# Kernel optimization log

Measured on AMD Instinct MI355X. Metric: run time of the kernel, lower is better.

## Reference

```python
import jax, jax.numpy as jnp
import numpy as np

N_NODES = 100000
N_EDGES = 500000
IN_DIM = 128
OUT_DIM = 128
NUM_HEADS = 4
HEAD_DIM = OUT_DIM // NUM_HEADS  # 32


def setup_inputs() -> dict:
    key = jax.random.key(0)
    k1, k2, k3, k4, k5, k6 = jax.random.split(key, 6)
    features = jax.random.normal(k1, (N_NODES, IN_DIM), dtype=jnp.float32)
    edge_index = jax.random.randint(k2, (2, N_EDGES), 0, N_NODES, dtype=jnp.int64)
    W_lin = jax.random.normal(k3, (OUT_DIM, IN_DIM), dtype=jnp.float32) * 0.05
    b_lin = jax.random.normal(k4, (OUT_DIM,), dtype=jnp.float32) * 0.05
    W_att = jax.random.normal(k5, (NUM_HEADS, 2 * OUT_DIM), dtype=jnp.float32) * 0.05
    b_att = jax.random.normal(k6, (NUM_HEADS,), dtype=jnp.float32) * 0.05
    return {"features": features, "edge_index": edge_index,
            "W_lin": W_lin, "b_lin": b_lin, "W_att": W_att, "b_att": b_att}


def reference(features, edge_index, W_lin, b_lin, W_att, b_att):
    num_nodes = features.shape[0]
    h = features @ W_lin.T + b_lin                     # [N, D]
    src, dst = edge_index[0], edge_index[1]
    src_h = h[src]                                     # [E, D]
    dst_h = h[dst]                                     # [E, D]
    # attention = Linear(cat([src_h, dst_h])) without materializing the concat
    logits = src_h @ W_att[:, :OUT_DIM].T + dst_h @ W_att[:, OUT_DIM:].T + b_att  # [E, H]
    # original softmaxes over dim=0 (all edges), per head
    attn = jax.nn.softmax(logits, axis=0)              # [E, H]
    # FAITHFUL quirk: only the first head_dim columns of src_h feed every head
    msgs = src_h[:, None, :HEAD_DIM] * attn[:, :, None]  # [E, H, head_dim]
    agg = jax.ops.segment_sum(msgs.reshape(msgs.shape[0], -1), dst,
                              num_segments=num_nodes)  # [N, H*head_dim] head-major
    return agg + h                                     # dropout(p=0) is identity
```

## Files before the change

### kernel.cpp

```cpp
#include <hip/hip_runtime.h>
#include <hip/hip_bf16.h>
#include <stdint.h>

#define N_NODES  100000
#define N_EDGES  500000
#define DIM      128
#define NUM_HEADS 4
#define HEAD_DIM  32
#define CAP      28

#define C_BLOCKS ((N_EDGES + 255) / 256)

typedef __attribute__((ext_vector_type(8))) __bf16 bf16x8;
typedef __attribute__((ext_vector_type(4))) __bf16 bf16x4;
typedef __attribute__((ext_vector_type(4))) float  f32x4;

__device__ __forceinline__ bf16x8 cvt8(const float* __restrict__ p)
{
    const float4 lo = *reinterpret_cast<const float4*>(p);
    const float4 hi = *reinterpret_cast<const float4*>(p + 4);
    bf16x8 r;
    r[0] = (__bf16)lo.x; r[1] = (__bf16)lo.y; r[2] = (__bf16)lo.z; r[3] = (__bf16)lo.w;
    r[4] = (__bf16)hi.x; r[5] = (__bf16)hi.y; r[6] = (__bf16)hi.z; r[7] = (__bf16)hi.w;
    return r;
}

__device__ __forceinline__ unsigned pack2_bf16(float a, float b)
{
    const __bf16 ba = (__bf16)a, bb = (__bf16)b;
    const unsigned short ua = __builtin_bit_cast(unsigned short, ba);
    const unsigned short ub = __builtin_bit_cast(unsigned short, bb);
    return (unsigned)ua | ((unsigned)ub << 16);
}

__device__ __forceinline__ float unpack_bf16(unsigned p, int hi)
{
    const unsigned short u = (unsigned short)(hi ? (p >> 16) : p);
    const __bf16 b = __builtin_bit_cast(__bf16, u);
    return (float)b;
}

__global__ __launch_bounds__(256) void cvt_wlin_kernel(
    const float* __restrict__ Wlin,
    __bf16* __restrict__ wb)
{
    const int i = blockIdx.x * 256 + threadIdx.x;
    const float4 v = *reinterpret_cast<const float4*>(Wlin + (size_t)i * 4);
    bf16x4 o;
    o[0] = (__bf16)v.x; o[1] = (__bf16)v.y; o[2] = (__bf16)v.z; o[3] = (__bf16)v.w;
    *reinterpret_cast<bf16x4*>(wb + (size_t)i * 4) = o;
}

__global__ __launch_bounds__(256) void gemm_dots_kernel(
    const float* __restrict__ feat,
    const __bf16* __restrict__ wb,
    const float* __restrict__ blin,
    const float* __restrict__ Watt,
    float* __restrict__ h,
    __bf16* __restrict__ h32,
    float* __restrict__ a_src,
    float* __restrict__ a_dst)
{
    __shared__ float wl[1280];
    const int tid = threadIdx.x;
#pragma unroll
    for (int i = 0; i < 4; ++i) {
        const int t  = tid + i * 256;
        const int hd = t >> 8;
        const int cf = t & 255;
        const int c  = cf & 127;
        const int df = cf >> 7;
        wl[c * 10 + df * 4 + hd] = Watt[t];
    }
    __syncthreads();

    const int wv   = tid >> 6;
    const int lane = tid & 63;
    const int wave = blockIdx.x * 4 + wv;
    const int m    = lane & 15;
    const int quad = lane >> 4;
    const int node0 = wave * 16;
    if (node0 >= N_NODES) return;

    f32x4 acc[8];
#pragma unroll
    for (int jt = 0; jt < 8; ++jt) acc[jt] = (f32x4){0.f, 0.f, 0.f, 0.f};

#pragma unroll
    for (int kc = 0; kc < 4; ++kc) {
        bf16x8 a = cvt8(feat + (size_t)(node0 + m) * DIM + kc * 32 + quad * 8);
#pragma unroll
        for (int jt = 0; jt < 8; ++jt) {
            bf16x8 b = *reinterpret_cast<const bf16x8*>(
                wb + ((jt * 16 + m) << 7) + kc * 32 + quad * 8);
            acc[jt] = __builtin_amdgcn_mfma_f32_16x16x32_bf16(a, b, acc[jt], 0, 0, 0);
        }
    }

    float dsrc[16], ddst[16];
#pragma unroll
    for (int i = 0; i < 16; ++i) { dsrc[i] = 0.f; ddst[i] = 0.f; }

#pragma unroll
    for (int jt = 0; jt < 8; ++jt) {
        const int col = jt * 16 + m;
        const float bl = blin[col];
        float w[8];
        *reinterpret_cast<float2*>(&w[0]) = *reinterpret_cast<const float2*>(&wl[col * 10 + 0]);
        *reinterpret_cast<float2*>(&w[2]) = *reinterpret_cast<const float2*>(&wl[col * 10 + 2]);
        *reinterpret_cast<float2*>(&w[4]) = *reinterpret_cast<const float2*>(&wl[col * 10 + 4]);
        *reinterpret_cast<float2*>(&w[6]) = *reinterpret_cast<const float2*>(&wl[col * 10 + 6]);
#pragma unroll
        for (int r = 0; r < 4; ++r) {
            const float hv = acc[jt][r] + bl;
            const int row = node0 + quad * 4 + r;
            h[(size_t)row * DIM + col] = hv;
            if (jt < 2)
                h32[(size_t)row * HEAD_DIM + col] = (__bf16)hv;
            dsrc[r * 4 + 0] += hv * w[0];
            dsrc[r * 4 + 1] += hv * w[1];
            dsrc[r * 4 + 2] += hv * w[2];
            dsrc[r * 4 + 3] += hv * w[3];
            ddst[r * 4 + 0] += hv * w[4];
            ddst[r * 4 + 1] += hv * w[5];
            ddst[r * 4 + 2] += hv * w[6];
            ddst[r * 4 + 3] += hv * w[7];
        }
    }

#pragma unroll
    for (int off = 1; off <= 8; off <<= 1) {
#pragma unroll
        for (int i = 0; i < 16; ++i) {
            dsrc[i] += __shfl_xor(dsrc[i], off, 64);
            ddst[i] += __shfl_xor(ddst[i], off, 64);
        }
    }
    if (m == 0) {
#pragma unroll
        for (int r = 0; r < 4; ++r) {
            const int node = node0 + quad * 4 + r;
            float4 s = {dsrc[r * 4 + 0], dsrc[r * 4 + 1], dsrc[r * 4 + 2], dsrc[r * 4 + 3]};
            float4 d = {ddst[r * 4 + 0], ddst[r * 4 + 1], ddst[r * 4 + 2], ddst[r * 4 + 3]};
            *reinterpret_cast<float4*>(a_src + (size_t)node * 4) = s;
            *reinterpret_cast<float4*>(a_dst + (size_t)node * 4) = d;
        }
    }
}

__global__ __launch_bounds__(256) void edge_exp_bucket_kernel(
    const int* __restrict__ ei,
    const float* __restrict__ a_src,
    const float* __restrict__ a_dst,
    const float* __restrict__ batt,
    float* __restrict__ partials,
    int* __restrict__ cursor,
    int4* __restrict__ slots)
{
    __shared__ float lds[4][4];
    const int e = blockIdx.x * 256 + threadIdx.x;
    const int wv = threadIdx.x >> 6;
    const int lane = threadIdx.x & 63;
    float ex0 = 0.f, ex1 = 0.f, ex2 = 0.f, ex3 = 0.f;
    if (e < N_EDGES) {
        const int s = ei[e];
        const int d = ei[N_EDGES + e];
        const float4 as = *reinterpret_cast<const float4*>(a_src + (size_t)s * 4);
        const float4 ad = *reinterpret_cast<const float4*>(a_dst + (size_t)d * 4);
        ex0 = __expf(as.x + ad.x + batt[0]);
        ex1 = __expf(as.y + ad.y + batt[1]);
        ex2 = __expf(as.z + ad.z + batt[2]);
        ex3 = __expf(as.w + ad.w + batt[3]);
        const int pos = atomicAdd(&cursor[d], 1);
        if (pos < CAP) {
            int4 q;
            q.x = s;
            q.y = (int)pack2_bf16(ex0, ex1);
            q.z = (int)pack2_bf16(ex2, ex3);
            q.w = 0;
            slots[(size_t)d * CAP + pos] = q;
        }
    }
#pragma unroll
    for (int off = 32; off > 0; off >>= 1) {
        ex0 += __shfl_xor(ex0, off, 64);
        ex1 += __shfl_xor(ex1, off, 64);
        ex2 += __shfl_xor(ex2, off, 64);
        ex3 += __shfl_xor(ex3, off, 64);
    }
    if (lane == 0) {
        lds[wv][0] = ex0; lds[wv][1] = ex1; lds[wv][2] = ex2; lds[wv][3] = ex3;
    }
    __syncthreads();
    if (threadIdx.x < 4) {
        const float s = lds[0][threadIdx.x] + lds[1][threadIdx.x]
                      + lds[2][threadIdx.x] + lds[3][threadIdx.x];
        atomicAdd(&partials[(blockIdx.x & 7) * 4 + threadIdx.x], s);
    }
}

__global__ __launch_bounds__(256) void aggregate_kernel(
    const float* __restrict__ h,
    const __bf16* __restrict__ h32,
    const float* __restrict__ partials,
    const int* __restrict__ cursor,
    const int4* __restrict__ slots,
    float* __restrict__ out)
{
    const int nv = blockIdx.x * 4 + (threadIdx.x >> 6);
    const int lane = threadIdx.x & 63;
    if (nv >= N_NODES) return;
    const int n = __builtin_amdgcn_readfirstlane(nv);

    const int hd0 = lane >> 5;
    const int dd  = lane & 31;

    const float hn0 = h[(size_t)n * DIM + lane];
    const float hn1 = h[(size_t)n * DIM + 64 + lane];
    const int cnt_raw = cursor[n];

    const float4* __restrict__ p4 = reinterpret_cast<const float4*>(partials);
    float Sx = 0.f, Sy = 0.f, Sz = 0.f, Sw = 0.f;
#pragma unroll
    for (int b = 0; b < 8; ++b) {
        const float4 t = p4[b];
        Sx += t.x; Sy += t.y; Sz += t.z; Sw += t.w;
    }
    const float inv0 = 1.0f / (hd0 ? Sy : Sx);
    const float inv1 = 1.0f / (hd0 ? Sw : Sz);

    const int cnt = cnt_raw > CAP ? CAP : cnt_raw;
    const int4* __restrict__ sl = slots + (size_t)n * CAP;

    float acc0 = 0.f, acc1 = 0.f;
    int j = 0;
    for (; j + 4 <= cnt; j += 4) {
        const int4 q0 = sl[j];
        const int4 q1 = sl[j + 1];
        const int4 q2 = sl[j + 2];
        const int4 q3 = sl[j + 3];
        const float v0 = (float)h32[(size_t)q0.x * HEAD_DIM + dd];
        const float v1 = (float)h32[(size_t)q1.x * HEAD_DIM + dd];
        const float v2 = (float)h32[(size_t)q2.x * HEAD_DIM + dd];
        const float v3 = (float)h32[(size_t)q3.x * HEAD_DIM + dd];
        acc0 += v0 * unpack_bf16((unsigned)q0.y, hd0);
        acc1 += v0 * unpack_bf16((unsigned)q0.z, hd0);
        acc0 += v1 * unpack_bf16((unsigned)q1.y, hd0);
        acc1 += v1 * unpack_bf16((unsigned)q1.z, hd0);
        acc0 += v2 * unpack_bf16((unsigned)q2.y, hd0);
        acc1 += v2 * unpack_bf16((unsigned)q2.z, hd0);
        acc0 += v3 * unpack_bf16((unsigned)q3.y, hd0);
        acc1 += v3 * unpack_bf16((unsigned)q3.z, hd0);
    }
    for (; j < cnt; ++j) {
        const int4 q = sl[j];
        const float v = (float)h32[(size_t)q.x * HEAD_DIM + dd];
        acc0 += v * unpack_bf16((unsigned)q.y, hd0);
        acc1 += v * unpack_bf16((unsigned)q.z, hd0);
    }
    out[(size_t)n * DIM + lane]      = acc0 * inv0 + hn0;
    out[(size_t)n * DIM + 64 + lane] = acc1 * inv1 + hn1;
}

extern "C" void kernel_launch(void* const* d_in, const int* in_sizes, int n_in,
                              void* d_out, int out_size, void* d_ws, size_t ws_size,
                              hipStream_t stream)
{
    const float* feat = (const float*)d_in[0];
    const int*   ei   = (const int*)d_in[1];
    const float* Wlin = (const float*)d_in[2];
    const float* blin = (const float*)d_in[3];
    const float* Watt = (const float*)d_in[4];
    const float* batt = (const float*)d_in[5];
    float*       out  = (float*)d_out;

    const size_t NF = (size_t)N_NODES * DIM;
    float*  h        = (float*)d_ws;
    float*  a_src    = h + NF;
    float*  a_dst    = a_src + (size_t)N_NODES * 4;
    int*    cursor   = (int*)(a_dst + (size_t)N_NODES * 4);
    float*  partials = (float*)(cursor + N_NODES);
    int4*   slots    = (int4*)(partials + 32);
    __bf16* h32      = (__bf16*)(slots + (size_t)N_NODES * CAP);
    __bf16* wlin_bf  = h32 + (size_t)N_NODES * HEAD_DIM;

    hipMemsetAsync(cursor, 0, (size_t)N_NODES * sizeof(int) + 32 * sizeof(float), stream);

    cvt_wlin_kernel<<<16, 256, 0, stream>>>(Wlin, wlin_bf);
    gemm_dots_kernel<<<1563, 256, 0, stream>>>(feat, wlin_bf, blin, Watt,
                                               h, h32, a_src, a_dst);
    edge_exp_bucket_kernel<<<C_BLOCKS, 256, 0, stream>>>(ei, a_src, a_dst, batt,
                                                         partials, cursor, slots);
    aggregate_kernel<<<25000, 256, 0, stream>>>(h, h32, partials, cursor, slots, out);
}
```

Measured before the change: 210.9 us.

## Restructure linear-layer GEMM with fragment-ordered weights and transposed MFMA output

The bf16 weight conversion now writes W_lin in the exact MFMA fragment order, so each lane loads one contiguous bf16x8 per tile. Each 16-node group is split across two waves that each compute half of the output columns. The MFMA operands are swapped so each lane holds four consecutive columns of a single node, which allows float4 stores of h and bf16x4 stores of h32 instead of scattered scalar stores. The attention dot reductions shrink to two shuffles plus an LDS combine across the two waves, at the cost of an extra block barrier and twice as many waves per node.

```diff
diff --git a/kernel.cpp b/kernel.cpp
--- a/kernel.cpp
+++ b/kernel.cpp
@@ -10,6 +10,7 @@
 #define CAP      28
 
 #define C_BLOCKS ((N_EDGES + 255) / 256)
+#define G_BLOCKS (N_NODES / 32)
 
 typedef __attribute__((ext_vector_type(8))) __bf16 bf16x8;
 typedef __attribute__((ext_vector_type(4))) __bf16 bf16x4;
@@ -44,11 +45,13 @@
     const float* __restrict__ Wlin,
     __bf16* __restrict__ wb)
 {
-    const int i = blockIdx.x * 256 + threadIdx.x;
-    const float4 v = *reinterpret_cast<const float4*>(Wlin + (size_t)i * 4);
-    bf16x4 o;
-    o[0] = (__bf16)v.x; o[1] = (__bf16)v.y; o[2] = (__bf16)v.z; o[3] = (__bf16)v.w;
-    *reinterpret_cast<bf16x4*>(wb + (size_t)i * 4) = o;
+    const int t    = blockIdx.x * 256 + threadIdx.x;
+    const int jt   = t >> 8;
+    const int kc   = (t >> 6) & 3;
+    const int quad = (t >> 4) & 3;
+    const int m    = t & 15;
+    const bf16x8 o = cvt8(Wlin + (size_t)(jt * 16 + m) * DIM + kc * 32 + quad * 8);
+    *reinterpret_cast<bf16x8*>(wb + (size_t)t * 8) = o;
 }
 
 __global__ __launch_bounds__(256) void gemm_dots_kernel(
@@ -62,6 +65,8 @@
     float* __restrict__ a_dst)
 {
     __shared__ float wl[1280];
+    __shared__ float bl_l[128];
+    __shared__ float sm[2][2][16][8];
     const int tid = threadIdx.x;
 #pragma unroll
     for (int i = 0; i < 4; ++i) {
@@ -72,79 +77,96 @@
         const int df = cf >> 7;
         wl[c * 10 + df * 4 + hd] = Watt[t];
     }
+    if (tid < 128) bl_l[tid] = blin[tid];
     __syncthreads();
 
     const int wv   = tid >> 6;
+    const int g    = wv >> 1;
+    const int ch   = wv & 1;
     const int lane = tid & 63;
-    const int wave = blockIdx.x * 4 + wv;
     const int m    = lane & 15;
     const int quad = lane >> 4;
-    const int node0 = wave * 16;
-    if (node0 >= N_NODES) return;
-
-    f32x4 acc[8];
-#pragma unroll
-    for (int jt = 0; jt < 8; ++jt) acc[jt] = (f32x4){0.f, 0.f, 0.f, 0.f};
+    const int node0 = (blockIdx.x * 2 + g) * 16;
+    const int node  = node0 + m;
+
+    f32x4 acc[4];
+#pragma unroll
+    for (int jtl = 0; jtl < 4; ++jtl) acc[jtl] = (f32x4){0.f, 0.f, 0.f, 0.f};
+
+    const bf16x8* __restrict__ wf =
+        reinterpret_cast<const bf16x8*>(wb) + (size_t)ch * 16 * 64 + lane;
 
 #pragma unroll
     for (int kc = 0; kc < 4; ++kc) {
-        bf16x8 a = cvt8(feat + (size_t)(node0 + m) * DIM + kc * 32 + quad * 8);
-#pragma unroll
-        for (int jt = 0; jt < 8; ++jt) {
-            bf16x8 b = *reinterpret_cast<const bf16x8*>(
-                wb + ((jt * 16 + m) << 7) + kc * 32 + quad * 8);
-            acc[jt] = __builtin_amdgcn_mfma_f32_16x16x32_bf16(a, b, acc[jt], 0, 0, 0);
-        }
-    }
-
-    float dsrc[16], ddst[16];
-#pragma unroll
-    for (int i = 0; i < 16; ++i) { dsrc[i] = 0.f; ddst[i] = 0.f; }
-
-#pragma unroll
-    for (int jt = 0; jt < 8; ++jt) {
-        const int col = jt * 16 + m;
-        const float bl = blin[col];
-        float w[8];
-        *reinterpret_cast<float2*>(&w[0]) = *reinterpret_cast<const float2*>(&wl[col * 10 + 0]);
-        *reinterpret_cast<float2*>(&w[2]) = *reinterpret_cast<const float2*>(&wl[col * 10 + 2]);
-        *reinterpret_cast<float2*>(&w[4]) = *reinterpret_cast<const float2*>(&wl[col * 10 + 4]);
-        *reinterpret_cast<float2*>(&w[6]) = *reinterpret_cast<const float2*>(&wl[col * 10 + 6]);
+        const bf16x8 a = cvt8(feat + (size_t)node * DIM + kc * 32 + quad * 8);
+#pragma unroll
+        for (int jtl = 0; jtl < 4; ++jtl) {
+            const bf16x8 b = wf[(jtl * 4 + kc) * 64];
+            acc[jtl] = __builtin_amdgcn_mfma_f32_16x16x32_bf16(b, a, acc[jtl], 0, 0, 0);
+        }
+    }
+
+    float dsrc[4] = {0.f, 0.f, 0.f, 0.f};
+    float ddst[4] = {0.f, 0.f, 0.f, 0.f};
+
+#pragma unroll
+    for (int jtl = 0; jtl < 4; ++jtl) {
+        const int jtg  = ch * 4 + jtl;
+        const int col0 = jtg * 16 + quad * 4;
+        const float4 bl4 = *reinterpret_cast<const float4*>(&bl_l[col0]);
+        float w[40];
+#pragma unroll
+        for (int k = 0; k < 10; ++k)
+            *reinterpret_cast<float4*>(&w[k * 4]) =
+                *reinterpret_cast<const float4*>(&wl[col0 * 10 + k * 4]);
+
+        float hv[4];
+        hv[0] = acc[jtl][0] + bl4.x;
+        hv[1] = acc[jtl][1] + bl4.y;
+        hv[2] = acc[jtl][2] + bl4.z;
+        hv[3] = acc[jtl][3] + bl4.w;
+
+        const float4 st = {hv[0], hv[1], hv[2], hv[3]};
+        *reinterpret_cast<float4*>(h + (size_t)node * DIM + col0) = st;
+        if (jtg < 2) {
+            bf16x4 o;
+            o[0] = (__bf16)hv[0]; o[1] = (__bf16)hv[1];
+            o[2] = (__bf16)hv[2]; o[3] = (__bf16)hv[3];
+            *reinterpret_cast<bf16x4*>(h32 + (size_t)node * HEAD_DIM + col0) = o;
+        }
 #pragma unroll
         for (int r = 0; r < 4; ++r) {
-            const float hv = acc[jt][r] + bl;
-            const int row = node0 + quad * 4 + r;
-            h[(size_t)row * DIM + col] = hv;
-            if (jt < 2)
-                h32[(size_t)row * HEAD_DIM + col] = (__bf16)hv;
-            dsrc[r * 4 + 0] += hv * w[0];
-            dsrc[r * 4 + 1] += hv * w[1];
-            dsrc[r * 4 + 2] += hv * w[2];
-            dsrc[r * 4 + 3] += hv * w[3];
-            ddst[r * 4 + 0] += hv * w[4];
-            ddst[r * 4 + 1] += hv * w[5];
-            ddst[r * 4 + 2] += hv * w[6];
-            ddst[r * 4 + 3] += hv * w[7];
-        }
-    }
-
-#pragma unroll
-    for (int off = 1; off <= 8; off <<= 1) {
-#pragma unroll
-        for (int i = 0; i < 16; ++i) {
+#pragma unroll
+            for (int hd = 0; hd < 4; ++hd) {
+                dsrc[hd] += hv[r] * w[r * 10 + hd];
+                ddst[hd] += hv[r] * w[r * 10 + 4 + hd];
+            }
+        }
+    }
+
+#pragma unroll
+    for (int off = 16; off <= 32; off <<= 1) {
+#pragma unroll
+        for (int i = 0; i < 4; ++i) {
             dsrc[i] += __shfl_xor(dsrc[i], off, 64);
             ddst[i] += __shfl_xor(ddst[i], off, 64);
         }
     }
-    if (m == 0) {
-#pragma unroll
-        for (int r = 0; r < 4; ++r) {
-            const int node = node0 + quad * 4 + r;
-            float4 s = {dsrc[r * 4 + 0], dsrc[r * 4 + 1], dsrc[r * 4 + 2], dsrc[r * 4 + 3]};
-            float4 d = {ddst[r * 4 + 0], ddst[r * 4 + 1], ddst[r * 4 + 2], ddst[r * 4 + 3]};
-            *reinterpret_cast<float4*>(a_src + (size_t)node * 4) = s;
-            *reinterpret_cast<float4*>(a_dst + (size_t)node * 4) = d;
-        }
+    if (quad == 0) {
+#pragma unroll
+        for (int i = 0; i < 4; ++i) {
+            sm[g][ch][m][i]     = dsrc[i];
+            sm[g][ch][m][4 + i] = ddst[i];
+        }
+    }
+    __syncthreads();
+    if (ch == 0 && quad == 0) {
+        const float4 s = {dsrc[0] + sm[g][1][m][0], dsrc[1] + sm[g][1][m][1],
+                          dsrc[2] + sm[g][1][m][2], dsrc[3] + sm[g][1][m][3]};
+        const float4 d = {ddst[0] + sm[g][1][m][4], ddst[1] + sm[g][1][m][5],
+                          ddst[2] + sm[g][1][m][6], ddst[3] + sm[g][1][m][7]};
+        *reinterpret_cast<float4*>(a_src + (size_t)node * 4) = s;
+        *reinterpret_cast<float4*>(a_dst + (size_t)node * 4) = d;
     }
 }
 
@@ -286,9 +308,9 @@
 
     hipMemsetAsync(cursor, 0, (size_t)N_NODES * sizeof(int) + 32 * sizeof(float), stream);
 
-    cvt_wlin_kernel<<<16, 256, 0, stream>>>(Wlin, wlin_bf);
-    gemm_dots_kernel<<<1563, 256, 0, stream>>>(feat, wlin_bf, blin, Watt,
-                                               h, h32, a_src, a_dst);
+    cvt_wlin_kernel<<<8, 256, 0, stream>>>(Wlin, wlin_bf);
+    gemm_dots_kernel<<<G_BLOCKS, 256, 0, stream>>>(feat, wlin_bf, blin, Watt,
+                                                   h, h32, a_src, a_dst);
     edge_exp_bucket_kernel<<<C_BLOCKS, 256, 0, stream>>>(ei, a_src, a_dst, batt,
                                                          partials, cursor, slots);
     aggregate_kernel<<<25000, 256, 0, stream>>>(h, h32, partials, cursor, slots, out);
```

Result: faster. 202.8 us (-3.8%).
